# Kernel optimization log

Measured on AMD Instinct MI355X. Metric: run time of the kernel, lower is better.

The kernel has to match this reference:

```python
import jax, jax.numpy as jnp
import numpy as np

B, Q, P, K, E, H = 2, 2500, 2500, 2500, 256, 8
D = E // H
FF = 2 * E
EPS = 1e-5


def layernorm(x, g, b):
    mu = jnp.mean(x, axis=-1, keepdims=True)
    var = jnp.var(x, axis=-1, keepdims=True)
    return (x - mu) * jax.lax.rsqrt(var + EPS) * g + b


def mha(q_in, k_in, v_in, wq, wk, wv, scale):
    n, ql = q_in.shape[0], q_in.shape[1]
    q = (q_in @ wq).reshape(n, ql, H, D)
    k = (k_in @ wk).reshape(n, k_in.shape[1], H, D)
    v = (v_in @ wv).reshape(n, v_in.shape[1], H, D)
    scores = jnp.einsum('nqhd,nkhd->nhqk', q, k) / scale
    attn = jax.nn.softmax(scores, axis=-1)
    return jnp.einsum('nhqk,nkhd->nqhd', attn, v).reshape(n, ql, E)


def setup_inputs() -> dict:
    key = jax.random.key(0)
    ks = jax.random.split(key, 24)
    s = lambda i, shape, sc=0.02: jax.random.normal(ks[i], shape, dtype=jnp.float32) * sc
    return {
        'prev_seq': jax.random.normal(ks[0], (B, P, E), dtype=jnp.float32),
        'query': jax.random.normal(ks[1], (B, Q, E), dtype=jnp.float32),
        'img_ft': jax.random.normal(ks[2], (B, K, E), dtype=jnp.float32),
        't_wq': s(3, (E, E)), 't_wk': s(4, (E, E)), 't_wv': s(5, (E, E)),
        's_wq': s(6, (E, E)), 's_wk': s(7, (E, E)), 's_wv': s(8, (E, E)),
        's_wo': s(9, (E, E)), 's_bo': jnp.zeros((E,), jnp.float32),
        'n1_g': jnp.ones((E,), jnp.float32), 'n1_b': jnp.zeros((E,), jnp.float32),
        'n2_g': jnp.ones((E,), jnp.float32), 'n2_b': jnp.zeros((E,), jnp.float32),
        'n3_g': jnp.ones((E,), jnp.float32), 'n3_b': jnp.zeros((E,), jnp.float32),
        'ff_w1': s(10, (E, FF)), 'ff_b1': jnp.zeros((FF,), jnp.float32),
        'ff_w2': s(11, (FF, E)), 'ff_b2': jnp.zeros((E,), jnp.float32),
    }


def reference(prev_seq, query, img_ft, t_wq, t_wk, t_wv, s_wq, s_wk, s_wv,
              s_wo, s_bo, n1_g, n1_b, n2_g, n2_b, n3_g, n3_b,
              ff_w1, ff_b1, ff_w2, ff_b2):
    # Temporal self-attention: K/V from prev_seq, scale = sqrt(embed_size)
    attn = mha(query, prev_seq, prev_seq, t_wq, t_wk, t_wv, float(E) ** 0.5)
    x = layernorm(attn + query, n1_g, n1_b)
    # Spatial cross-attention: K/V from img_ft, scale = sqrt(head_dim), with fc_out
    cross = mha(x, img_ft, img_ft, s_wq, s_wk, s_wv, float(D) ** 0.5)
    cross = cross @ s_wo + s_bo
    x = layernorm(cross + x, n2_g, n2_b)
    # FFN: E -> 2E -> ReLU -> E
    ff = jax.nn.relu(x @ ff_w1 + ff_b1) @ ff_w2 + ff_b2
    return layernorm(ff + x, n3_g, n3_b)
```

## Files before the change

kernel.cpp:

```cpp
#include <hip/hip_runtime.h>
#include <hip/hip_bf16.h>
#include <stdint.h>


typedef __bf16 bf16_t;
typedef __bf16 bf16x8 __attribute__((ext_vector_type(8)));
typedef __bf16 bf16x4 __attribute__((ext_vector_type(4)));
typedef float  f32x4  __attribute__((ext_vector_type(4)));
typedef float  f32x16 __attribute__((ext_vector_type(16)));
typedef uint32_t u32;
typedef uint32_t u32x4 __attribute__((ext_vector_type(4)));

#define NB   2
#define SEQ  2500
#define EMB  256
#define NH   8
#define HD   32
#define MTOT (NB*SEQ)
#define KVSPLIT 3
#define SPLITLEN 834
#define NPAIR 14

static __device__ __forceinline__ f32x4 mfma16(bf16x8 a, bf16x8 b, f32x4 c) {
  return __builtin_amdgcn_mfma_f32_16x16x32_bf16(a, b, c, 0, 0, 0);
}
static __device__ __forceinline__ f32x16 mfma32(bf16x8 a, bf16x8 b, f32x16 c) {
  return __builtin_amdgcn_mfma_f32_32x32x16_bf16(a, b, c, 0, 0, 0);
}
static __device__ __forceinline__ u32 pack2(float a, float b) {
  union { __bf16 h; unsigned short s; } x, y;
  x.h = (__bf16)a; y.h = (__bf16)b;
  return (u32)x.s | ((u32)y.s << 16);
}

__global__ __launch_bounds__(256) void prep_kernel(
    const float* s0, const float* s1, const float* s2, const float* s3,
    const float* s4, const float* s5, const float* s6, const float* s7,
    const float* s8, bf16_t* wt,
    const float* aq, const float* ap, const float* ai,
    bf16_t* dq, bf16_t* dp, bf16_t* di)
{
  int b = blockIdx.x;
  if (b < 176) {
    const float* src; int R, C, tl; size_t doff;
    if (b < 112) {
      int mi = b >> 4; tl = b & 15; R = 256; C = 256; doff = (size_t)mi * 65536;
      switch (mi) {
        case 0: src = s0; break; case 1: src = s1; break; case 2: src = s2; break;
        case 3: src = s3; break; case 4: src = s4; break; case 5: src = s5; break;
        default: src = s6;
      }
    } else if (b < 144) { tl = b - 112; R = 256; C = 512; doff = 458752; src = s7; }
    else                { tl = b - 144; R = 512; C = 256; doff = 589824; src = s8; }
    const int tpr = C >> 6;
    const int tr = tl / tpr, tc = tl % tpr;
    bf16_t* dst = wt + doff;
    #pragma unroll
    for (int i = 0; i < 16; ++i) {
      int lin = i * 256 + threadIdx.x;
      int lr = lin >> 6, lc = lin & 63;
      int rr = tr * 64 + lr, cc = tc * 64 + lc;
      dst[(size_t)cc * R + rr] = (__bf16)src[(size_t)rr * C + cc];
    }
    return;
  }
  int idx = b - 176;
  int t = idx / 313, r = idx % 313;
  const float* src = (t == 0) ? aq : (t == 1) ? ap : ai;
  bf16_t* dst = (t == 0) ? dq : (t == 1) ? dp : di;
  #pragma unroll
  for (int k = 0; k < 4; ++k) {
    int i = r * 1024 + k * 256 + threadIdx.x;
    if (i < 320000) {
      float4 v = ((const float4*)src)[i];
      bf16x4 o;
      o[0] = (__bf16)v.x; o[1] = (__bf16)v.y; o[2] = (__bf16)v.z; o[3] = (__bf16)v.w;
      ((bf16x4*)dst)[i] = o;
    }
  }
}

template<int K>
static __device__ __forceinline__ void gemm32_body(
    const bf16_t* __restrict__ A, const bf16_t* __restrict__ Wt,
    const float* __restrict__ bias, bf16_t* __restrict__ Cout,
    int M, int N, int relu, float cscale, int bx, int by)
{
  const int tid = threadIdx.x;
  const int lane = tid & 63, wid = tid >> 6;
  const int l31 = lane & 31, hi = lane >> 5;
  const int mbase = bx * 128 + wid * 32;
  const int nbase = by * 64;

  int arow = mbase + l31; if (arow > M - 1) arow = M - 1;
  const bf16_t* ap = A + (size_t)arow * K + hi * 8;
  const bf16_t* bp = Wt + (size_t)(nbase + l31) * K + hi * 8;

  f32x16 acc0 = {}, acc1 = {};
  #pragma unroll
  for (int kk = 0; kk < K; kk += 16) {
    bf16x8 a  = *(const bf16x8*)(ap + kk);
    bf16x8 b0 = *(const bf16x8*)(bp + kk);
    bf16x8 b1 = *(const bf16x8*)(bp + (size_t)32 * K + kk);
    acc0 = mfma32(a, b0, acc0);
    acc1 = mfma32(a, b1, acc1);
  }
  #pragma unroll
  for (int r = 0; r < 16; ++r) {
    const int row = mbase + (r & 3) + ((r >> 2) << 3) + hi * 4;
    if (row < M) {
      const int c0 = nbase + l31;
      const int c1 = nbase + 32 + l31;
      float v0 = acc0[r] * cscale + (bias ? bias[c0] : 0.f);
      float v1 = acc1[r] * cscale + (bias ? bias[c1] : 0.f);
      if (relu) { v0 = fmaxf(v0, 0.f); v1 = fmaxf(v1, 0.f); }
      Cout[(size_t)row * N + c0] = (bf16_t)v0;
      Cout[(size_t)row * N + c1] = (bf16_t)v1;
    }
  }
}

__global__ __launch_bounds__(256) void gemm_relu_kernel(
    const bf16_t* __restrict__ A, const bf16_t* __restrict__ Wt,
    const float* __restrict__ bias, bf16_t* __restrict__ Cout,
    int M, int N)
{
  gemm32_body<256>(A, Wt, bias, Cout, M, N, 1, 1.f, blockIdx.x, blockIdx.y);
}

__global__ __launch_bounds__(256) void proj3_kernel(
    const bf16_t* A0, const bf16_t* W0, bf16_t* C0,
    const bf16_t* A1, const bf16_t* W1, bf16_t* C1,
    const bf16_t* A2, const bf16_t* W2, bf16_t* C2, float qsc)
{
  const bf16_t* A = (blockIdx.z == 0) ? A0 : (blockIdx.z == 1) ? A1 : A2;
  const bf16_t* W = (blockIdx.z == 0) ? W0 : (blockIdx.z == 1) ? W1 : W2;
  bf16_t* C = (blockIdx.z == 0) ? C0 : (blockIdx.z == 1) ? C1 : C2;
  const float cs = (blockIdx.z == 0) ? qsc : 1.f;
  gemm32_body<256>(A, W, nullptr, C, MTOT, 256, 0, cs, blockIdx.x, blockIdx.y);
}

template<int K>
__global__ __launch_bounds__(256) void gemm_ln_kernel(
    const bf16_t* __restrict__ A, const bf16_t* __restrict__ Wt,
    const float* __restrict__ bias, const bf16_t* __restrict__ resid,
    const float* __restrict__ gw, const float* __restrict__ bw,
    bf16_t* __restrict__ OutB, float* __restrict__ OutF, int M)
{
  __shared__ float red[16][4][2];
  const int tid = threadIdx.x;
  const int lane = tid & 63, wid = tid >> 6;
  const int l15 = lane & 15, g = lane >> 4;
  const int mbase = blockIdx.x * 16;
  const int nbase = wid * 64;

  int arow = mbase + l15; if (arow > M - 1) arow = M - 1;
  const bf16_t* ap = A + (size_t)arow * K + g * 8;
  const bf16_t* bp = Wt + (size_t)(nbase + l15) * K + g * 8;

  f32x4 acc[4];
  #pragma unroll
  for (int j = 0; j < 4; ++j) acc[j] = (f32x4){0.f,0.f,0.f,0.f};

  #pragma unroll
  for (int kk = 0; kk < K; kk += 32) {
    bf16x8 a = *(const bf16x8*)(ap + kk);
    #pragma unroll
    for (int ct = 0; ct < 4; ++ct) {
      bf16x8 bfr = *(const bf16x8*)(bp + (size_t)ct * 16 * K + kk);
      acc[ct] = mfma16(a, bfr, acc[ct]);
    }
  }

  float x[4][4];
  float xs[4] = {0.f,0.f,0.f,0.f}, xq[4] = {0.f,0.f,0.f,0.f};
  #pragma unroll
  for (int ct = 0; ct < 4; ++ct) {
    const int col = nbase + ct * 16 + l15;
    const float bv = bias[col];
    #pragma unroll
    for (int r = 0; r < 4; ++r) {
      int row = mbase + g * 4 + r; if (row > M - 1) row = M - 1;
      float v = acc[ct][r] + bv + (float)resid[(size_t)row * EMB + col];
      x[ct][r] = v;
      xs[r] += v; xq[r] += v * v;
    }
  }
  #pragma unroll
  for (int r = 0; r < 4; ++r) {
    #pragma unroll
    for (int m = 1; m < 16; m <<= 1) {
      xs[r] += __shfl_xor(xs[r], m);
      xq[r] += __shfl_xor(xq[r], m);
    }
  }
  if (l15 == 0) {
    #pragma unroll
    for (int r = 0; r < 4; ++r) {
      red[g * 4 + r][wid][0] = xs[r];
      red[g * 4 + r][wid][1] = xq[r];
    }
  }
  __syncthreads();
  #pragma unroll
  for (int r = 0; r < 4; ++r) {
    const int rl = g * 4 + r;
    const float S = red[rl][0][0] + red[rl][1][0] + red[rl][2][0] + red[rl][3][0];
    const float Q = red[rl][0][1] + red[rl][1][1] + red[rl][2][1] + red[rl][3][1];
    const float mean = S * (1.f / EMB);
    const float var = Q * (1.f / EMB) - mean * mean;
    const float rstd = rsqrtf(var + 1e-5f);
    const int row = mbase + rl;
    if (row < M) {
      #pragma unroll
      for (int ct = 0; ct < 4; ++ct) {
        const int col = nbase + ct * 16 + l15;
        const float y = (x[ct][r] - mean) * rstd * gw[col] + bw[col];
        if (OutF) OutF[(size_t)row * EMB + col] = y;
        else      OutB[(size_t)row * EMB + col] = (bf16_t)y;
      }
    }
  }
}

__global__ __launch_bounds__(256, 2) void attn_part_kernel(
    const bf16_t* __restrict__ Qm, const bf16_t* __restrict__ Km,
    const bf16_t* __restrict__ Vm, bf16_t* __restrict__ Op,
    float* __restrict__ Lp)
{
  __shared__ bf16_t Vt[4][32][40];

  const int tid = threadIdx.x;
  const int lane = tid & 63, wid = tid >> 6;
  const int q32 = lane & 31, hi = lane >> 5;

  const int n = blockIdx.x;
  const int vid = (n & 7) * 60 + (n >> 3);
  const int grp = vid / 10;
  const int sub = vid - grp * 10;
  const int bh = grp / 3;
  const int split = grp - bh * 3;

  const size_t qoff = (size_t)(bh >> 3) * SEQ * EMB + (bh & 7) * HD;
  const int kv_begin = split * SPLITLEN;
  const int kv_end = min(kv_begin + SPLITLEN, SEQ);

  const int qbase = sub * 256 + wid * 64;
  const int qrX = min(qbase + q32, SEQ - 1);
  const int qrY = min(qbase + 32 + q32, SEQ - 1);
  const bf16x8 qfaX = *(const bf16x8*)(Qm + qoff + (size_t)qrX * EMB + hi * 8);
  const bf16x8 qfbX = *(const bf16x8*)(Qm + qoff + (size_t)qrX * EMB + 16 + hi * 8);
  const bf16x8 qfaY = *(const bf16x8*)(Qm + qoff + (size_t)qrY * EMB + hi * 8);
  const bf16x8 qfbY = *(const bf16x8*)(Qm + qoff + (size_t)qrY * EMB + 16 + hi * 8);

  f32x16 accAX = {}, accBX = {}, accAY = {}, accBY = {};
  float lsumX = 0.f, lsumY = 0.f;

  const int skv = tid >> 3;
  const int sd0 = (tid & 7) << 2;
  const int scc = (skv + ((sd0 >> 3) << 3)) & 31;

  const bf16_t* kp = Km + qoff + (size_t)(kv_begin + q32) * EMB + hi * 8;
  const bf16_t* vp = Vm + qoff + (size_t)(kv_begin + skv) * EMB + sd0;

  bf16x4 vA = *(const bf16x4*)vp;
  bf16x4 vB = *(const bf16x4*)(vp + 32 * EMB);
  bf16x8 kaA = *(const bf16x8*)kp;
  bf16x8 kbA = *(const bf16x8*)(kp + 16);
  bf16x8 kaB = *(const bf16x8*)(kp + 32 * EMB);
  bf16x8 kbB = *(const bf16x8*)(kp + 32 * EMB + 16);
  kp += 64 * EMB;
  vp += 64 * EMB;

#define TREE16(dst, p)                                                         \
    {                                                                          \
      float t0 = p[0] + p[1],  t1 = p[2] + p[3];                               \
      float t2 = p[4] + p[5],  t3 = p[6] + p[7];                               \
      float t4 = p[8] + p[9],  t5 = p[10] + p[11];                             \
      float t6 = p[12] + p[13], t7 = p[14] + p[15];                            \
      float u0 = t0 + t1, u1 = t2 + t3, u2 = t4 + t5, u3 = t6 + t7;            \
      dst = (u0 + u1) + (u2 + u3);                                             \
    }

#define SOFTPACK(p, f1, f2)                                                    \
    {                                                                          \
      u32 w0 = pack2(p[0], p[1]),   w1 = pack2(p[2], p[3]);                    \
      u32 w2 = pack2(p[4], p[5]),   w3 = pack2(p[6], p[7]);                    \
      u32 w4 = pack2(p[8], p[9]),   w5 = pack2(p[10], p[11]);                  \
      u32 w6 = pack2(p[12], p[13]), w7 = pack2(p[14], p[15]);                  \
      asm("v_permlane32_swap_b32 %0, %1" : "+v"(w0), "+v"(w2));                \
      asm("v_permlane32_swap_b32 %0, %1" : "+v"(w1), "+v"(w3));                \
      asm("v_permlane32_swap_b32 %0, %1" : "+v"(w4), "+v"(w6));                \
      asm("v_permlane32_swap_b32 %0, %1" : "+v"(w5), "+v"(w7));                \
      f1.x = w0; f1.y = w1; f1.z = w2; f1.w = w3;                              \
      f2.x = w4; f2.y = w5; f2.z = w6; f2.w = w7;                              \
    }

#define EXPALL(p, s) _Pragma("unroll")                                         \
    for (int r = 0; r < 16; ++r) p[r] = __builtin_amdgcn_exp2f(s[r]);

#define MASKT(p, kv0)                                                          \
    {                                                                          \
      _Pragma("unroll")                                                        \
      for (int r = 0; r < 16; ++r) {                                           \
        const int kvg = (kv0) + (r & 3) + ((r >> 2) << 3) + hi * 4;            \
        if (kvg >= kv_end) p[r] = 0.f;                                         \
      }                                                                        \
    }

#define ATTN_PAIR(P, MASKED, PREFETCH)                                         \
  {                                                                            \
    const int bufA = ((P) & 1) << 1, bufB = bufA + 1;                          \
    _Pragma("unroll")                                                          \
    for (int j = 0; j < 4; ++j) {                                              \
      Vt[bufA][sd0 + j][scc] = vA[j];                                          \
      Vt[bufB][sd0 + j][scc] = vB[j];                                          \
    }                                                                          \
    bf16x4 vAn, vBn; bf16x8 kaAn, kbAn, kaBn, kbBn;                            \
    if (PREFETCH) {                                                            \
      vAn = *(const bf16x4*)vp;                                                \
      vBn = *(const bf16x4*)(vp + 32 * EMB);                                   \
      kaAn = *(const bf16x8*)kp;                                               \
      kbAn = *(const bf16x8*)(kp + 16);                                        \
      kaBn = *(const bf16x8*)(kp + 32 * EMB);                                  \
      kbBn = *(const bf16x8*)(kp + 32 * EMB + 16);                             \
      kp += 64 * EMB; vp += 64 * EMB;                                          \
    }                                                                          \
    f32x16 sAX = {}, sBX = {}, sAY = {}, sBY = {};                             \
    sAX = mfma32(kaA, qfaX, sAX);                                              \
    sBX = mfma32(kaB, qfaX, sBX);                                              \
    sAY = mfma32(kaA, qfaY, sAY);                                              \
    sBY = mfma32(kaB, qfaY, sBY);                                              \
    sAX = mfma32(kbA, qfbX, sAX);                                              \
    sBX = mfma32(kbB, qfbX, sBX);                                              \
    sAY = mfma32(kbA, qfbY, sAY);                                              \
    sBY = mfma32(kbB, qfbY, sBY);                                              \
    float pAX[16], pBX[16], pAY[16], pBY[16];                                  \
    EXPALL(pAX, sAX) EXPALL(pBX, sBX) EXPALL(pAY, sAY) EXPALL(pBY, sBY)        \
    if (MASKED) {                                                              \
      const int kvA = kv_begin + (((P) << 1) << 5);                            \
      const int kvB = kvA + 32;                                                \
      MASKT(pAX, kvA) MASKT(pAY, kvA) MASKT(pBX, kvB) MASKT(pBY, kvB)          \
    }                                                                          \
    float ps0, ps1, ps2, ps3;                                                  \
    TREE16(ps0, pAX) TREE16(ps1, pBX) TREE16(ps2, pAY) TREE16(ps3, pBY)        \
    lsumX += ps0 + ps1; lsumY += ps2 + ps3;                                    \
    u32x4 f1AX, f2AX, f1BX, f2BX, f1AY, f2AY, f1BY, f2BY;                      \
    SOFTPACK(pAX, f1AX, f2AX)                                                  \
    SOFTPACK(pBX, f1BX, f2BX)                                                  \
    SOFTPACK(pAY, f1AY, f2AY)                                                  \
    SOFTPACK(pBY, f1BY, f2BY)                                                  \
    __syncthreads();                                                           \
    const int c1 = ((hi + (q32 >> 3)) & 3) << 3;                               \
    const int c2 = ((2 + hi + (q32 >> 3)) & 3) << 3;                           \
    bf16x8 vf1A = *(const bf16x8*)&Vt[bufA][q32][c1];                          \
    bf16x8 vf2A = *(const bf16x8*)&Vt[bufA][q32][c2];                          \
    bf16x8 vf1B = *(const bf16x8*)&Vt[bufB][q32][c1];                          \
    bf16x8 vf2B = *(const bf16x8*)&Vt[bufB][q32][c2];                          \
    accAX = mfma32(*(bf16x8*)&f1AX, vf1A, accAX);                              \
    accBX = mfma32(*(bf16x8*)&f1BX, vf1B, accBX);                              \
    accAY = mfma32(*(bf16x8*)&f1AY, vf1A, accAY);                              \
    accBY = mfma32(*(bf16x8*)&f1BY, vf1B, accBY);                              \
    accAX = mfma32(*(bf16x8*)&f2AX, vf2A, accAX);                              \
    accBX = mfma32(*(bf16x8*)&f2BX, vf2B, accBX);                              \
    accAY = mfma32(*(bf16x8*)&f2AY, vf2A, accAY);                              \
    accBY = mfma32(*(bf16x8*)&f2BY, vf2B, accBY);                              \
    if (PREFETCH) {                                                            \
      kaA = kaAn; kbA = kbAn; kaB = kaBn; kbB = kbBn;                          \
      vA = vAn; vB = vBn;                                                      \
    }                                                                          \
  }

  #pragma unroll
  for (int P = 0; P < NPAIR - 1; ++P) ATTN_PAIR(P, 0, 1)
  ATTN_PAIR(NPAIR - 1, 1, 0)
#undef ATTN_PAIR
#undef SOFTPACK
#undef TREE16
#undef EXPALL
#undef MASKT

  lsumX += __shfl_xor(lsumX, 32);
  lsumY += __shfl_xor(lsumY, 32);
  const size_t pbase = ((size_t)split * 16 + bh) * SEQ;
  #pragma unroll
  for (int r = 0; r < 16; ++r) {
    const int qX = qbase + (r & 3) + ((r >> 2) << 3) + hi * 4;
    const int qY = qX + 32;
    if (qX < SEQ) Op[(pbase + qX) * 32 + q32] = (bf16_t)(accAX[r] + accBX[r]);
    if (qY < SEQ) Op[(pbase + qY) * 32 + q32] = (bf16_t)(accAY[r] + accBY[r]);
  }
  if (lane < 32) {
    const int qX = qbase + lane, qY = qX + 32;
    if (qX < SEQ) Lp[pbase + qX] = lsumX;
    if (qY < SEQ) Lp[pbase + qY] = lsumY;
  }
}

__global__ __launch_bounds__(256) void merge_kernel(
    const bf16_t* __restrict__ Op, const float* __restrict__ Lp,
    const bf16_t* __restrict__ resid, const float* __restrict__ gw,
    const float* __restrict__ bw, bf16_t* __restrict__ out, int doLN)
{
  const int lane = threadIdx.x & 63, wid = threadIdx.x >> 6;
  const int row = blockIdx.x * 4 + wid;
  const int b = row / SEQ, q = row - b * SEQ;
  const int h = lane >> 3, dl = (lane & 7) * 4;
  const int bh = b * 8 + h;

  float L = 0.f;
  float acc[4] = {0.f, 0.f, 0.f, 0.f};
  #pragma unroll
  for (int s = 0; s < KVSPLIT; ++s) {
    const size_t pb = ((size_t)s * 16 + bh) * SEQ + q;
    L += Lp[pb];
    bf16x4 ov = *(const bf16x4*)(Op + pb * 32 + dl);
    #pragma unroll
    for (int j = 0; j < 4; ++j) acc[j] += (float)ov[j];
  }
  const float invL = 1.f / L;
  const size_t base = (size_t)row * EMB + lane * 4;
  if (!doLN) {
    bf16x4 ov;
    #pragma unroll
    for (int j = 0; j < 4; ++j) ov[j] = (__bf16)(acc[j] * invL);
    *(bf16x4*)(out + base) = ov;
    return;
  }
  bf16x4 rv = *(const bf16x4*)(resid + base);
  float x[4], s = 0.f, sq = 0.f;
  #pragma unroll
  for (int j = 0; j < 4; ++j) {
    x[j] = acc[j] * invL + (float)rv[j];
    s += x[j]; sq += x[j] * x[j];
  }
  #pragma unroll
  for (int m = 1; m < 64; m <<= 1) { s += __shfl_xor(s, m); sq += __shfl_xor(sq, m); }
  const float mean = s * (1.f / EMB);
  const float var = sq * (1.f / EMB) - mean * mean;
  const float rstd = rsqrtf(var + 1e-5f);
  float4 gv = *(const float4*)(gw + lane * 4);
  float4 bv = *(const float4*)(bw + lane * 4);
  bf16x4 ov;
  ov[0] = (__bf16)((x[0] - mean) * rstd * gv.x + bv.x);
  ov[1] = (__bf16)((x[1] - mean) * rstd * gv.y + bv.y);
  ov[2] = (__bf16)((x[2] - mean) * rstd * gv.z + bv.z);
  ov[3] = (__bf16)((x[3] - mean) * rstd * gv.w + bv.w);
  *(bf16x4*)(out + base) = ov;
}

extern "C" void kernel_launch(void* const* d_in, const int* in_sizes, int n_in,
                              void* d_out, int out_size, void* d_ws, size_t ws_size,
                              hipStream_t stream)
{
  (void)in_sizes; (void)n_in; (void)out_size; (void)ws_size;
  const float* prev  = (const float*)d_in[0];
  const float* query = (const float*)d_in[1];
  const float* img   = (const float*)d_in[2];
  const float* t_wq  = (const float*)d_in[3];
  const float* t_wk  = (const float*)d_in[4];
  const float* t_wv  = (const float*)d_in[5];
  const float* s_wq  = (const float*)d_in[6];
  const float* s_wk  = (const float*)d_in[7];
  const float* s_wv  = (const float*)d_in[8];
  const float* s_wo  = (const float*)d_in[9];
  const float* s_bo  = (const float*)d_in[10];
  const float* n1g = (const float*)d_in[11];
  const float* n1b = (const float*)d_in[12];
  const float* n2g = (const float*)d_in[13];
  const float* n2b = (const float*)d_in[14];
  const float* n3g = (const float*)d_in[15];
  const float* n3b = (const float*)d_in[16];
  const float* ffw1 = (const float*)d_in[17];
  const float* ffb1 = (const float*)d_in[18];
  const float* ffw2 = (const float*)d_in[19];
  const float* ffb2 = (const float*)d_in[20];

  bf16_t* ws   = (bf16_t*)d_ws;
  bf16_t* WT   = ws;
  bf16_t* WTF1 = ws + 458752;
  bf16_t* WTF2 = ws + 589824;
  bf16_t* qbf = ws + 720896;
  bf16_t* pbf = qbf + 1280000;
  bf16_t* ibf = pbf + 1280000;
  bf16_t* qb = ibf + 1280000;
  bf16_t* kb = qb + 1280000;
  bf16_t* vb = kb + 1280000;
  bf16_t* ab = vb + 1280000;
  bf16_t* x1 = ab + 1280000;
  bf16_t* cb = x1 + 1280000;
  bf16_t* x2 = cb + 1280000;
  bf16_t* hb = x2 + 1280000;
  bf16_t* fb = hb + 2560000;
  float* outp = (float*)d_out;
  bf16_t* Op = cb;
  float*  Lp = (float*)pbf;

  const float log2e = 1.4426950408889634f;
  const float qscT = log2e * (1.f / 16.f);
  const float qscS = log2e * 0.17677669529663687f;

  dim3 blk(256);
  prep_kernel<<<1115, blk, 0, stream>>>(t_wq, t_wk, t_wv, s_wq, s_wk, s_wv,
                                        s_wo, ffw1, ffw2, ws,
                                        query, prev, img, qbf, pbf, ibf);

  dim3 gP(40, 4, 3), gG512(40, 8);
  proj3_kernel<<<gP, blk, 0, stream>>>(qbf, WT, qb,
                                       pbf, WT + 65536, kb,
                                       pbf, WT + 131072, vb, qscT);
  attn_part_kernel<<<480, blk, 0, stream>>>(qb, kb, vb, Op, Lp);
  merge_kernel<<<1250, blk, 0, stream>>>(Op, Lp, qbf, n1g, n1b, x1, 1);
  proj3_kernel<<<gP, blk, 0, stream>>>(x1,  WT + 196608, qb,
                                       ibf, WT + 262144, kb,
                                       ibf, WT + 327680, vb, qscS);
  attn_part_kernel<<<480, blk, 0, stream>>>(qb, kb, vb, Op, Lp);
  merge_kernel<<<1250, blk, 0, stream>>>(Op, Lp, nullptr, nullptr, nullptr, ab, 0);
  gemm_ln_kernel<256><<<313, blk, 0, stream>>>(ab, WT + 393216, s_bo, x1,
                                               n2g, n2b, x2, nullptr, MTOT);
  gemm_relu_kernel<<<gG512, blk, 0, stream>>>(x2, WTF1, ffb1, hb, MTOT, 512);
  gemm_ln_kernel<512><<<313, blk, 0, stream>>>(hb, WTF2, ffb2, x2,
                                               n3g, n3b, nullptr, outp, MTOT);
  (void)fb;
}
```

Measured before the change: 164.9 us.

## Hoist spatial K/V projections into first launch and fuse merge into fc_out GEMM

```diff
diff --git a/kernel.cpp b/kernel.cpp
--- a/kernel.cpp
+++ b/kernel.cpp
@@ -128,16 +128,128 @@
   gemm32_body<256>(A, Wt, bias, Cout, M, N, 1, 1.f, blockIdx.x, blockIdx.y);
 }
 
-__global__ __launch_bounds__(256) void proj3_kernel(
-    const bf16_t* A0, const bf16_t* W0, bf16_t* C0,
-    const bf16_t* A1, const bf16_t* W1, bf16_t* C1,
-    const bf16_t* A2, const bf16_t* W2, bf16_t* C2, float qsc)
-{
-  const bf16_t* A = (blockIdx.z == 0) ? A0 : (blockIdx.z == 1) ? A1 : A2;
-  const bf16_t* W = (blockIdx.z == 0) ? W0 : (blockIdx.z == 1) ? W1 : W2;
-  bf16_t* C = (blockIdx.z == 0) ? C0 : (blockIdx.z == 1) ? C1 : C2;
-  const float cs = (blockIdx.z == 0) ? qsc : 1.f;
+__global__ __launch_bounds__(256) void proj5_kernel(
+    const bf16_t* qbf, const bf16_t* pbf, const bf16_t* ibf,
+    const bf16_t* WT,
+    bf16_t* tq, bf16_t* tk, bf16_t* tv, bf16_t* sk, bf16_t* sv, float qsc)
+{
+  const int z = blockIdx.z;
+  const bf16_t* A; const bf16_t* W; bf16_t* C; float cs = 1.f;
+  switch (z) {
+    case 0:  A = qbf; W = WT;          C = tq; cs = qsc; break;
+    case 1:  A = pbf; W = WT + 65536;  C = tk; break;
+    case 2:  A = pbf; W = WT + 131072; C = tv; break;
+    case 3:  A = ibf; W = WT + 262144; C = sk; break;
+    default: A = ibf; W = WT + 327680; C = sv; break;
+  }
   gemm32_body<256>(A, W, nullptr, C, MTOT, 256, 0, cs, blockIdx.x, blockIdx.y);
+}
+
+__global__ __launch_bounds__(256) void projq_kernel(
+    const bf16_t* __restrict__ A, const bf16_t* __restrict__ W,
+    bf16_t* __restrict__ C, float sc)
+{
+  gemm32_body<256>(A, W, nullptr, C, MTOT, 256, 0, sc, blockIdx.x, blockIdx.y);
+}
+
+__global__ __launch_bounds__(256) void gemm_ln_merge_kernel(
+    const bf16_t* __restrict__ Op0, const bf16_t* __restrict__ Op1,
+    const bf16_t* __restrict__ Op2, const float* __restrict__ Lp,
+    const bf16_t* __restrict__ Wt, const float* __restrict__ bias,
+    const bf16_t* __restrict__ resid, const float* __restrict__ gw,
+    const float* __restrict__ bw, bf16_t* __restrict__ OutB, int M)
+{
+  __shared__ float red[16][4][2];
+  const int tid = threadIdx.x;
+  const int lane = tid & 63, wid = tid >> 6;
+  const int l15 = lane & 15, g = lane >> 4;
+  const int mbase = blockIdx.x * 16;
+  const int nbase = wid * 64;
+
+  int arow = mbase + l15; if (arow > M - 1) arow = M - 1;
+  const int b = arow / SEQ, q = arow - b * SEQ;
+
+  float invLh[8];
+  #pragma unroll
+  for (int h = 0; h < 8; ++h) {
+    const size_t lb = (size_t)(b * 8 + h) * SEQ + q;
+    invLh[h] = 1.f / (Lp[lb] + Lp[lb + (size_t)16 * SEQ]
+                              + Lp[lb + (size_t)32 * SEQ]);
+  }
+  const size_t ob0 = ((size_t)(b * 8) * SEQ + q) * 32 + g * 8;
+  const bf16_t* bp = Wt + (size_t)(nbase + l15) * 256 + g * 8;
+
+  f32x4 acc[4];
+  #pragma unroll
+  for (int j = 0; j < 4; ++j) acc[j] = (f32x4){0.f,0.f,0.f,0.f};
+
+  #pragma unroll
+  for (int kk = 0; kk < 256; kk += 32) {
+    const int h = kk >> 5;
+    const size_t ob = ob0 + (size_t)h * (SEQ * 32);
+    bf16x8 o0 = *(const bf16x8*)(Op0 + ob);
+    bf16x8 o1 = *(const bf16x8*)(Op1 + ob);
+    bf16x8 o2 = *(const bf16x8*)(Op2 + ob);
+    const float inv = invLh[h];
+    bf16x8 a;
+    #pragma unroll
+    for (int j = 0; j < 8; ++j)
+      a[j] = (__bf16)(((float)o0[j] + (float)o1[j] + (float)o2[j]) * inv);
+    #pragma unroll
+    for (int ct = 0; ct < 4; ++ct) {
+      bf16x8 bfr = *(const bf16x8*)(bp + (size_t)ct * 16 * 256 + kk);
+      acc[ct] = mfma16(a, bfr, acc[ct]);
+    }
+  }
+
+  float x[4][4];
+  float xs[4] = {0.f,0.f,0.f,0.f}, xq[4] = {0.f,0.f,0.f,0.f};
+  #pragma unroll
+  for (int ct = 0; ct < 4; ++ct) {
+    const int col = nbase + ct * 16 + l15;
+    const float bv = bias[col];
+    #pragma unroll
+    for (int r = 0; r < 4; ++r) {
+      int row = mbase + g * 4 + r; if (row > M - 1) row = M - 1;
+      float v = acc[ct][r] + bv + (float)resid[(size_t)row * EMB + col];
+      x[ct][r] = v;
+      xs[r] += v; xq[r] += v * v;
+    }
+  }
+  #pragma unroll
+  for (int r = 0; r < 4; ++r) {
+    #pragma unroll
+    for (int m = 1; m < 16; m <<= 1) {
+      xs[r] += __shfl_xor(xs[r], m);
+      xq[r] += __shfl_xor(xq[r], m);
+    }
+  }
+  if (l15 == 0) {
+    #pragma unroll
+    for (int r = 0; r < 4; ++r) {
+      red[g * 4 + r][wid][0] = xs[r];
+      red[g * 4 + r][wid][1] = xq[r];
+    }
+  }
+  __syncthreads();
+  #pragma unroll
+  for (int r = 0; r < 4; ++r) {
+    const int rl = g * 4 + r;
+    const float S = red[rl][0][0] + red[rl][1][0] + red[rl][2][0] + red[rl][3][0];
+    const float Q = red[rl][0][1] + red[rl][1][1] + red[rl][2][1] + red[rl][3][1];
+    const float mean = S * (1.f / EMB);
+    const float var = Q * (1.f / EMB) - mean * mean;
+    const float rstd = rsqrtf(var + 1e-5f);
+    const int row = mbase + rl;
+    if (row < M) {
+      #pragma unroll
+      for (int ct = 0; ct < 4; ++ct) {
+        const int col = nbase + ct * 16 + l15;
+        OutB[(size_t)row * EMB + col] =
+            (bf16_t)((x[ct][r] - mean) * rstd * gw[col] + bw[col]);
+      }
+    }
+  }
 }
 
 template<int K>
@@ -225,7 +337,8 @@
 
 __global__ __launch_bounds__(256, 2) void attn_part_kernel(
     const bf16_t* __restrict__ Qm, const bf16_t* __restrict__ Km,
-    const bf16_t* __restrict__ Vm, bf16_t* __restrict__ Op,
+    const bf16_t* __restrict__ Vm, bf16_t* __restrict__ Op0,
+    bf16_t* __restrict__ Op1, bf16_t* __restrict__ Op2,
     float* __restrict__ Lp)
 {
   __shared__ bf16_t Vt[4][32][40];
@@ -382,25 +495,28 @@
 
   lsumX += __shfl_xor(lsumX, 32);
   lsumY += __shfl_xor(lsumY, 32);
-  const size_t pbase = ((size_t)split * 16 + bh) * SEQ;
+  bf16_t* Opx = (split == 0) ? Op0 : (split == 1) ? Op1 : Op2;
+  const size_t obase = (size_t)bh * SEQ;
+  const size_t lbase = ((size_t)split * 16 + bh) * SEQ;
   #pragma unroll
   for (int r = 0; r < 16; ++r) {
     const int qX = qbase + (r & 3) + ((r >> 2) << 3) + hi * 4;
     const int qY = qX + 32;
-    if (qX < SEQ) Op[(pbase + qX) * 32 + q32] = (bf16_t)(accAX[r] + accBX[r]);
-    if (qY < SEQ) Op[(pbase + qY) * 32 + q32] = (bf16_t)(accAY[r] + accBY[r]);
+    if (qX < SEQ) Opx[(obase + qX) * 32 + q32] = (bf16_t)(accAX[r] + accBX[r]);
+    if (qY < SEQ) Opx[(obase + qY) * 32 + q32] = (bf16_t)(accAY[r] + accBY[r]);
   }
   if (lane < 32) {
     const int qX = qbase + lane, qY = qX + 32;
-    if (qX < SEQ) Lp[pbase + qX] = lsumX;
-    if (qY < SEQ) Lp[pbase + qY] = lsumY;
+    if (qX < SEQ) Lp[lbase + qX] = lsumX;
+    if (qY < SEQ) Lp[lbase + qY] = lsumY;
   }
 }
 
 __global__ __launch_bounds__(256) void merge_kernel(
-    const bf16_t* __restrict__ Op, const float* __restrict__ Lp,
+    const bf16_t* __restrict__ Op0, const bf16_t* __restrict__ Op1,
+    const bf16_t* __restrict__ Op2, const float* __restrict__ Lp,
     const bf16_t* __restrict__ resid, const float* __restrict__ gw,
-    const float* __restrict__ bw, bf16_t* __restrict__ out, int doLN)
+    const float* __restrict__ bw, bf16_t* __restrict__ out)
 {
   const int lane = threadIdx.x & 63, wid = threadIdx.x >> 6;
   const int row = blockIdx.x * 4 + wid;
@@ -408,30 +524,21 @@
   const int h = lane >> 3, dl = (lane & 7) * 4;
   const int bh = b * 8 + h;
 
-  float L = 0.f;
-  float acc[4] = {0.f, 0.f, 0.f, 0.f};
-  #pragma unroll
-  for (int s = 0; s < KVSPLIT; ++s) {
-    const size_t pb = ((size_t)s * 16 + bh) * SEQ + q;
-    L += Lp[pb];
-    bf16x4 ov = *(const bf16x4*)(Op + pb * 32 + dl);
-    #pragma unroll
-    for (int j = 0; j < 4; ++j) acc[j] += (float)ov[j];
-  }
+  const size_t lb = (size_t)bh * SEQ + q;
+  const float L = Lp[lb] + Lp[lb + (size_t)16 * SEQ] + Lp[lb + (size_t)32 * SEQ];
   const float invL = 1.f / L;
+
+  const size_t pb = ((size_t)bh * SEQ + q) * 32 + dl;
+  bf16x4 o0 = *(const bf16x4*)(Op0 + pb);
+  bf16x4 o1 = *(const bf16x4*)(Op1 + pb);
+  bf16x4 o2 = *(const bf16x4*)(Op2 + pb);
+
   const size_t base = (size_t)row * EMB + lane * 4;
-  if (!doLN) {
-    bf16x4 ov;
-    #pragma unroll
-    for (int j = 0; j < 4; ++j) ov[j] = (__bf16)(acc[j] * invL);
-    *(bf16x4*)(out + base) = ov;
-    return;
-  }
   bf16x4 rv = *(const bf16x4*)(resid + base);
   float x[4], s = 0.f, sq = 0.f;
   #pragma unroll
   for (int j = 0; j < 4; ++j) {
-    x[j] = acc[j] * invL + (float)rv[j];
+    x[j] = ((float)o0[j] + (float)o1[j] + (float)o2[j]) * invL + (float)rv[j];
     s += x[j]; sq += x[j] * x[j];
   }
   #pragma unroll
@@ -489,11 +596,17 @@
   bf16_t* ab = vb + 1280000;
   bf16_t* x1 = ab + 1280000;
   bf16_t* cb = x1 + 1280000;
-  bf16_t* x2 = cb + 1280000;
-  bf16_t* hb = x2 + 1280000;
+  bf16_t* x2r = cb + 1280000;
+  bf16_t* hb = x2r + 1280000;
   bf16_t* fb = hb + 2560000;
   float* outp = (float*)d_out;
-  bf16_t* Op = cb;
+
+  bf16_t* Op0 = ab;
+  bf16_t* Op1 = cb;
+  bf16_t* Op2 = x2r;
+  bf16_t* kb2 = hb;
+  bf16_t* vb2 = hb + 1280000;
+  bf16_t* X2 = vb;
   float*  Lp = (float*)pbf;
 
   const float log2e = 1.4426950408889634f;
@@ -505,21 +618,18 @@
                                         s_wo, ffw1, ffw2, ws,
                                         query, prev, img, qbf, pbf, ibf);
 
-  dim3 gP(40, 4, 3), gG512(40, 8);
-  proj3_kernel<<<gP, blk, 0, stream>>>(qbf, WT, qb,
-                                       pbf, WT + 65536, kb,
-                                       pbf, WT + 131072, vb, qscT);
-  attn_part_kernel<<<480, blk, 0, stream>>>(qb, kb, vb, Op, Lp);
-  merge_kernel<<<1250, blk, 0, stream>>>(Op, Lp, qbf, n1g, n1b, x1, 1);
-  proj3_kernel<<<gP, blk, 0, stream>>>(x1,  WT + 196608, qb,
-                                       ibf, WT + 262144, kb,
-                                       ibf, WT + 327680, vb, qscS);
-  attn_part_kernel<<<480, blk, 0, stream>>>(qb, kb, vb, Op, Lp);
-  merge_kernel<<<1250, blk, 0, stream>>>(Op, Lp, nullptr, nullptr, nullptr, ab, 0);
-  gemm_ln_kernel<256><<<313, blk, 0, stream>>>(ab, WT + 393216, s_bo, x1,
-                                               n2g, n2b, x2, nullptr, MTOT);
-  gemm_relu_kernel<<<gG512, blk, 0, stream>>>(x2, WTF1, ffb1, hb, MTOT, 512);
-  gemm_ln_kernel<512><<<313, blk, 0, stream>>>(hb, WTF2, ffb2, x2,
+  dim3 gP5(40, 4, 5), gP1(40, 4), gG512(40, 8);
+  proj5_kernel<<<gP5, blk, 0, stream>>>(qbf, pbf, ibf, WT,
+                                        qb, kb, vb, kb2, vb2, qscT);
+  attn_part_kernel<<<480, blk, 0, stream>>>(qb, kb, vb, Op0, Op1, Op2, Lp);
+  merge_kernel<<<1250, blk, 0, stream>>>(Op0, Op1, Op2, Lp, qbf, n1g, n1b, x1);
+  projq_kernel<<<gP1, blk, 0, stream>>>(x1, WT + 196608, qb, qscS);
+  attn_part_kernel<<<480, blk, 0, stream>>>(qb, kb2, vb2, Op0, Op1, Op2, Lp);
+  gemm_ln_merge_kernel<<<313, blk, 0, stream>>>(Op0, Op1, Op2, Lp,
+                                                WT + 393216, s_bo, x1,
+                                                n2g, n2b, X2, MTOT);
+  gemm_relu_kernel<<<gG512, blk, 0, stream>>>(X2, WTF1, ffb1, hb, MTOT, 512);
+  gemm_ln_kernel<512><<<313, blk, 0, stream>>>(hb, WTF2, ffb2, X2,
                                                n3g, n3b, nullptr, outp, MTOT);
   (void)fb;
 }
```

After: 165.7 us. No clear change (+0.5%).
